# Performance work log

Hardware: AMD Instinct MI355X
Metric: run time of the kernel (lower is better)

## Reference

```python
import jax, jax.numpy as jnp
import numpy as np

DIM = 1024
HEADS = 16
DIM_HEAD = 64
INNER = HEADS * DIM_HEAD  # 1024
SCALE = DIM_HEAD ** -0.5


def setup_inputs() -> dict:
    key = jax.random.key(0)
    ks = jax.random.split(key, 5)
    B, N = 4, 2048
    x = jax.random.normal(ks[0], (B, N, DIM), dtype=jnp.float32)
    # torch Linear weights are [out, in]; store transposed [in, out] for x @ W
    s = 1.0 / np.sqrt(DIM)
    Wq = jax.random.uniform(ks[1], (DIM, INNER), minval=-s, maxval=s, dtype=jnp.float32)
    Wkv = jax.random.uniform(ks[2], (DIM, 2 * INNER), minval=-s, maxval=s, dtype=jnp.float32)
    so = 1.0 / np.sqrt(INNER)
    Wo = jax.random.uniform(ks[3], (INNER, DIM), minval=-so, maxval=so, dtype=jnp.float32)
    bo = jax.random.uniform(ks[4], (DIM,), minval=-so, maxval=so, dtype=jnp.float32)
    return {"x": x, "Wq": Wq, "Wkv": Wkv, "Wo": Wo, "bo": bo}


def reference(x, Wq, Wkv, Wo, bo):
    B, N, _ = x.shape
    q = x @ Wq                      # [B, N, INNER]
    kv = x @ Wkv                    # [B, N, 2*INNER]
    k, v = jnp.split(kv, 2, axis=-1)

    def split_heads(t):
        return t.reshape(B, N, HEADS, DIM_HEAD).transpose(0, 2, 1, 3)  # [B,H,N,D]

    q, k, v = split_heads(q) * SCALE, split_heads(k), split_heads(v)
    sim = jnp.einsum('bhid,bhjd->bhij', q, k)  # [B,H,N,N]
    mask_value = -jnp.finfo(sim.dtype).max
    # causal: mask strictly-upper triangle (triu with offset j-i+1 = 1)
    causal_mask = jnp.triu(jnp.ones((N, N), dtype=bool), k=1)
    sim = jnp.where(causal_mask[None, None, :, :], mask_value, sim)
    attn = jax.nn.softmax(sim, axis=-1)
    out = jnp.einsum('bhij,bhjd->bhid', attn, v)            # [B,H,N,D]
    out = out.transpose(0, 2, 1, 3).reshape(B, N, INNER)    # [B,N,INNER]
    return out @ Wo + bo
```

## Files before the change

kernel.cpp:

```cpp
#include <hip/hip_runtime.h>

typedef unsigned short u16;
typedef __bf16 bf16x8 __attribute__((ext_vector_type(8)));
typedef float floatx4 __attribute__((ext_vector_type(4)));
typedef unsigned as1_u32 __attribute__((address_space(1)));
typedef unsigned as3_u32 __attribute__((address_space(3)));

__device__ inline u16 f2bf(float f) {
    unsigned int u = __builtin_bit_cast(unsigned int, f);
    u += 0x7fffu + ((u >> 16) & 1u);
    return (u16)(u >> 16);
}
__device__ inline floatx4 mfma16(bf16x8 a, bf16x8 b, floatx4 c) {
    return __builtin_amdgcn_mfma_f32_16x16x32_bf16(a, b, c, 0, 0, 0);
}
__device__ inline void gld16(const u16* g, u16* l) {
    __builtin_amdgcn_global_load_lds((const as1_u32*)g, (as3_u32*)l, 16, 0, 0);
}
__device__ inline unsigned permpack(float lo, float hi) {
    return __builtin_amdgcn_perm(__builtin_bit_cast(unsigned, hi),
                                 __builtin_bit_cast(unsigned, lo), 0x07060302u);
}

#define NSEQ 2048
#define DIM  1024
#define HEADS 16
#define DHEAD 64
#define QSCALE 0.18033688f
#define CSHIFT 4.328085f

__device__ inline void transpose_tile(const float* __restrict__ src,
                                      u16* __restrict__ dst, int ncols,
                                      int n0, int k0, int t) {
    __shared__ u16 tile[64][72];
    #pragma unroll
    for (int rr = 0; rr < 4; rr++) {
        const int k = (t >> 4) + rr * 16;
        const int n = (t & 15) * 4;
        float4 v = *(const float4*)&src[(size_t)(k0 + k) * ncols + n0 + n];
        tile[n + 0][k] = f2bf(v.x); tile[n + 1][k] = f2bf(v.y);
        tile[n + 2][k] = f2bf(v.z); tile[n + 3][k] = f2bf(v.w);
    }
    __syncthreads();
    #pragma unroll
    for (int ww = 0; ww < 2; ww++) {
        const int idx = t + ww * 256;
        const int n = idx >> 3, g = idx & 7;
        u16 tmp[8] __attribute__((aligned(16)));
        #pragma unroll
        for (int i = 0; i < 8; i++) tmp[i] = tile[n][g * 8 + i];
        *(uint4*)&dst[(size_t)(n0 + n) * 1024 + k0 + g * 8] = *(const uint4*)tmp;
    }
}

__global__ __launch_bounds__(256) void prep_fused(
    const float* __restrict__ x,  u16* __restrict__ xb,
    const float* __restrict__ Wq, const float* __restrict__ Wkv,
    u16* __restrict__ Wt,
    const float* __restrict__ Wo, u16* __restrict__ WotF)
{
    const int bid = blockIdx.x;
    const int t = threadIdx.x;
    if (bid < 4096) {
        const size_t i = ((size_t)bid * 256 + t) * 8;
        float4 a = *(const float4*)&x[i];
        float4 b = *(const float4*)&x[i + 4];
        u16 o[8] __attribute__((aligned(16)));
        o[0] = f2bf(a.x); o[1] = f2bf(a.y); o[2] = f2bf(a.z); o[3] = f2bf(a.w);
        o[4] = f2bf(b.x); o[5] = f2bf(b.y); o[6] = f2bf(b.z); o[7] = f2bf(b.w);
        *(uint4*)&xb[i] = *(const uint4*)o;
    } else if (bid < 4352) {
        const int v = bid - 4096;
        transpose_tile(Wq, Wt, 1024, (v & 15) * 64, (v >> 4) * 64, t);
    } else if (bid < 4864) {
        const int v = bid - 4352;
        transpose_tile(Wkv, Wt + (size_t)1024 * 1024, 2048, (v & 31) * 64, (v >> 5) * 64, t);
    } else {
        const int v = bid - 4864;
        transpose_tile(Wo, WotF, 1024, (v & 15) * 64, (v >> 4) * 64, t);
    }
}

__global__ __launch_bounds__(256) void transpose_conv(const float* __restrict__ src,
                                                      u16* __restrict__ dst, int ncols) {
    transpose_tile(src, dst, ncols, blockIdx.x * 64, blockIdx.y * 64, threadIdx.x);
}

__global__ __launch_bounds__(256) void qkv_gemm_v6(
    const u16* __restrict__ xb, const u16* __restrict__ Wt,
    u16* __restrict__ q_ws, u16* __restrict__ k_ws, u16* __restrict__ v_ws)
{
    __shared__ u16 As[2][2][128 * 32];
    __shared__ u16 Bs[2][2][128 * 32];

    const int n0 = blockIdx.x * 128;
    const int m0 = blockIdx.y * 128;
    const int t = threadIdx.x, lane = t & 63, w = t >> 6;
    const int wr = w >> 1, wc = w & 1;
    const int quad = lane >> 4, l16 = lane & 15;
    const int lrow = lane >> 2;
    const int lk = (((lane & 3) ^ ((lane >> 3) & 3)) * 8);
    const int rsw = ((l16 >> 1) & 3);

    floatx4 acc[4][4];
    #pragma unroll
    for (int i = 0; i < 4; i++)
        #pragma unroll
        for (int j = 0; j < 4; j++) acc[i][j] = floatx4{0.f, 0.f, 0.f, 0.f};

#define STAGE_V6(kt, buf) do {                                             \
    const size_t k0s = (size_t)(kt) * 64;                                  \
    _Pragma("unroll")                                                      \
    for (int hh = 0; hh < 2; hh++) {                                       \
        const int row = w * 32 + hh * 16;                                  \
        const size_t ga = (size_t)(m0 + row + lrow) * DIM + k0s + lk;      \
        const size_t gb = (size_t)(n0 + row + lrow) * DIM + k0s + lk;      \
        gld16(&xb[ga],      &As[buf][0][row * 32]);                        \
        gld16(&xb[ga + 32], &As[buf][1][row * 32]);                        \
        gld16(&Wt[gb],      &Bs[buf][0][row * 32]);                        \
        gld16(&Wt[gb + 32], &Bs[buf][1][row * 32]);                        \
    }                                                                      \
} while (0)

    STAGE_V6(0, 0);
    STAGE_V6(1, 1);

    for (int kt = 0; kt < 16; kt++) {
        const int cur = kt & 1;
        if (kt < 15) asm volatile("s_waitcnt vmcnt(8)" ::: "memory");
        else         asm volatile("s_waitcnt vmcnt(0)" ::: "memory");
        __builtin_amdgcn_s_barrier();
        __builtin_amdgcn_sched_barrier(0);

        #pragma unroll
        for (int ks = 0; ks < 2; ks++) {
            const u16* al = &As[cur][ks][0];
            const u16* bl = &Bs[cur][ks][0];
            bf16x8 af[4], bf[4];
            #pragma unroll
            for (int i = 0; i < 4; i++)
                af[i] = *(const bf16x8*)&al[(wr * 64 + i * 16 + l16) * 32
                                            + ((quad ^ rsw) * 8)];
            #pragma unroll
            for (int j = 0; j < 4; j++)
                bf[j] = *(const bf16x8*)&bl[(wc * 64 + j * 16 + l16) * 32
                                            + ((quad ^ rsw) * 8)];
            __builtin_amdgcn_s_setprio(1);
            #pragma unroll
            for (int i = 0; i < 4; i++)
                #pragma unroll
                for (int j = 0; j < 4; j++)
                    acc[i][j] = mfma16(af[i], bf[j], acc[i][j]);
            __builtin_amdgcn_s_setprio(0);
        }

        __builtin_amdgcn_sched_barrier(0);
        __builtin_amdgcn_s_barrier();
        __builtin_amdgcn_sched_barrier(0);
        if (kt < 14) STAGE_V6(kt + 2, cur);
    }
#undef STAGE_V6

    const int seg = n0 >> 10;
    #pragma unroll
    for (int j = 0; j < 4; j++) {
        const int n  = n0 + wc * 64 + j * 16 + l16;
        const int nn = n & 1023;
        const int h  = nn >> 6, d = nn & 63;
        #pragma unroll
        for (int i = 0; i < 4; i++) {
            const int mb = m0 + wr * 64 + i * 16 + quad * 4;
            const int b = mb >> 11, ib = mb & (NSEQ - 1);
            if (seg == 0) {
                #pragma unroll
                for (int r = 0; r < 4; r++)
                    q_ws[(((size_t)(b * HEADS + h)) * NSEQ + ib + r) * DHEAD + d] =
                        f2bf(acc[i][j][r] * QSCALE);
            } else if (seg == 1) {
                #pragma unroll
                for (int r = 0; r < 4; r++)
                    k_ws[(((size_t)(b * HEADS + h)) * NSEQ + ib + r) * DHEAD + d] =
                        f2bf(acc[i][j][r]);
            } else {
                u16 tmp[4] __attribute__((aligned(8)));
                #pragma unroll
                for (int r = 0; r < 4; r++) tmp[r] = f2bf(acc[i][j][r]);
                *(uint2*)&v_ws[(((size_t)(b * HEADS + h)) * DHEAD + d) * NSEQ + ib] =
                    *(const uint2*)tmp;
            }
        }
    }
}

__global__ __launch_bounds__(256) void attn_v11(
    const u16* __restrict__ q_ws, const u16* __restrict__ k_ws,
    const u16* __restrict__ v_ws, u16* __restrict__ attn_ws)
{
    __shared__ u16 kds[2][64 * 64];
    __shared__ u16 vds[2][64 * 64];
    __shared__ u16 p_lds[4 * 1024];

    const int bid = blockIdx.x;
    const int bh  = bid & 63;
    const int pr  = bid >> 6;
    const int b   = bh >> 4, h = bh & 15;

    const u16* qb = q_ws + (size_t)bh * NSEQ * DHEAD;
    const u16* kb = k_ws + (size_t)bh * NSEQ * DHEAD;
    const u16* vb = v_ws + (size_t)bh * DHEAD * NSEQ;

    const int t    = threadIdx.x;
    const int lane = t & 63, w = t >> 6;
    const int quad = lane >> 4, l16 = lane & 15;

    const int srow8 = lane >> 3;
    const int chunk = (lane & 7) ^ srow8;
    const int krow  = w * 16 + srow8;
    const size_t koff = (size_t)krow * DHEAD + chunk * 8;
    const size_t voff = (size_t)krow * NSEQ + chunk * 8;
    u16* klbase = (u16*)&kds[0][0] + w * 1024;
    u16* vlbase = (u16*)&vds[0][0] + w * 1024;
    const int sw = (l16 & 7);

    bf16x8 ones;
    #pragma unroll
    for (int i = 0; i < 8; i++) ones[i] = (__bf16)1.0f;

    for (int seg = 0; seg < 2; seg++) {
        const int tq = seg ? pr : (31 - pr);
        const int i0 = tq * 64;
        const int jt_max = tq;

        bf16x8 qf[2];
        #pragma unroll
        for (int dg = 0; dg < 2; dg++)
            qf[dg] = *(const bf16x8*)&qb[(size_t)(i0 + w * 16 + l16) * DHEAD
                                         + dg * 32 + quad * 8];

        floatx4 lacc = floatx4{0.f, 0.f, 0.f, 0.f};
        floatx4 acc[4];
        #pragma unroll
        for (int dg = 0; dg < 4; dg++) acc[dg] = floatx4{0.f, 0.f, 0.f, 0.f};

        __syncthreads();
        gld16(&kb[koff],             klbase);
        gld16(&kb[koff + 8 * DHEAD], klbase + 512);
        gld16(&vb[voff],             vlbase);
        gld16(&vb[voff + 8 * NSEQ],  vlbase + 512);

        for (int jt = 0; jt <= jt_max; jt++) {
            const int cur = jt & 1;
            __syncthreads();

            if (jt < jt_max) {
                const size_t j64 = (size_t)(jt + 1) * 64;
                const int nb = (cur ^ 1) * 4096;
                gld16(&kb[j64 * DHEAD + koff],             klbase + nb);
                gld16(&kb[j64 * DHEAD + koff + 8 * DHEAD], klbase + nb + 512);
                gld16(&vb[j64 + voff],                     vlbase + nb);
                gld16(&vb[j64 + voff + 8 * NSEQ],          vlbase + nb + 512);
            }

            const u16* kl = &kds[cur][0];
            const u16* vl = &vds[cur][0];
            const int j0 = jt * 64;

            floatx4 s[4];
            #pragma unroll
            for (int g = 0; g < 4; g++)
                s[g] = floatx4{-CSHIFT, -CSHIFT, -CSHIFT, -CSHIFT};
            __builtin_amdgcn_s_setprio(1);
            #pragma unroll
            for (int dg = 0; dg < 2; dg++)
                #pragma unroll
                for (int g = 0; g < 4; g++) {
                    bf16x8 kf = *(const bf16x8*)&kl[(g * 16 + l16) * 64
                                                    + (((dg * 4 + quad) ^ sw) * 8)];
                    s[g] = mfma16(kf, qf[dg], s[g]);
                }
            __builtin_amdgcn_s_setprio(0);

            if (j0 + 63 > i0 + w * 16) {
                const int i = i0 + w * 16 + l16;
                #pragma unroll
                for (int g = 0; g < 4; g++) {
                    const int jb = j0 + g * 16 + quad * 4;
                    #pragma unroll
                    for (int r = 0; r < 4; r++)
                        if (jb + r > i) s[g][r] = -1e30f;
                }
            }

            #pragma unroll
            for (int g = 0; g < 4; g++) {
                #pragma unroll
                for (int r = 0; r < 4; r++)
                    s[g][r] = __builtin_amdgcn_exp2f(s[g][r]);
                uint2 pk;
                pk.x = permpack(s[g][0], s[g][1]);
                pk.y = permpack(s[g][2], s[g][3]);
                const int c = 2 * g + (quad >> 1);
                *(uint2*)&p_lds[w * 1024 + (c >> 2) * 512 + (c & 3) * 128
                                + l16 * 8 + (quad & 1) * 4] = pk;
            }
            asm volatile("s_waitcnt lgkmcnt(0)" ::: "memory");

            __builtin_amdgcn_s_setprio(1);
            #pragma unroll
            for (int jg = 0; jg < 2; jg++) {
                bf16x8 pf = *(const bf16x8*)&p_lds[w * 1024 + jg * 512
                                                   + quad * 128 + l16 * 8];
                lacc = mfma16(pf, ones, lacc);
                #pragma unroll
                for (int dg = 0; dg < 4; dg++) {
                    bf16x8 vf = *(const bf16x8*)&vl[(dg * 16 + l16) * 64
                                                    + (((jg * 4 + quad) ^ sw) * 8)];
                    acc[dg] = mfma16(pf, vf, acc[dg]);
                }
            }
            __builtin_amdgcn_s_setprio(0);
        }

        float linv[4];
        #pragma unroll
        for (int r = 0; r < 4; r++)
            linv[r] = 1.0f / lacc[r];
        #pragma unroll
        for (int dg = 0; dg < 4; dg++)
            #pragma unroll
            for (int r = 0; r < 4; r++) {
                const float o = acc[dg][r] * linv[r];
                const int i = i0 + w * 16 + quad * 4 + r;
                attn_ws[(((size_t)(b * NSEQ + i)) * HEADS + h) * DHEAD + dg * 16 + l16] =
                    f2bf(o);
            }
    }
}

__global__ __launch_bounds__(256) void out_gemm_v6(
    const u16* __restrict__ attn, const u16* __restrict__ Wot,
    const float* __restrict__ bo, float* __restrict__ out)
{
    __shared__ u16 As[2][2][128 * 32];
    __shared__ u16 Bs[2][2][128 * 32];

    const int n0 = blockIdx.x * 128;
    const int m0 = blockIdx.y * 128;
    const int t = threadIdx.x, lane = t & 63, w = t >> 6;
    const int wr = w >> 1, wc = w & 1;
    const int quad = lane >> 4, l16 = lane & 15;
    const int lrow = lane >> 2;
    const int lk = (((lane & 3) ^ ((lane >> 3) & 3)) * 8);
    const int rsw = ((l16 >> 1) & 3);

    floatx4 acc[4][4];
    #pragma unroll
    for (int i = 0; i < 4; i++)
        #pragma unroll
        for (int j = 0; j < 4; j++) acc[i][j] = floatx4{0.f, 0.f, 0.f, 0.f};

#define STAGE_O6(kt, buf) do {                                             \
    const size_t k0s = (size_t)(kt) * 64;                                  \
    _Pragma("unroll")                                                      \
    for (int hh = 0; hh < 2; hh++) {                                       \
        const int row = w * 32 + hh * 16;                                  \
        const size_t ga = (size_t)(m0 + row + lrow) * DIM + k0s + lk;      \
        const size_t gb = (size_t)(n0 + row + lrow) * DIM + k0s + lk;      \
        gld16(&attn[ga],      &As[buf][0][row * 32]);                      \
        gld16(&attn[ga + 32], &As[buf][1][row * 32]);                      \
        gld16(&Wot[gb],       &Bs[buf][0][row * 32]);                      \
        gld16(&Wot[gb + 32],  &Bs[buf][1][row * 32]);                      \
    }                                                                      \
} while (0)

    STAGE_O6(0, 0);
    STAGE_O6(1, 1);

    for (int kt = 0; kt < 16; kt++) {
        const int cur = kt & 1;
        if (kt < 15) asm volatile("s_waitcnt vmcnt(8)" ::: "memory");
        else         asm volatile("s_waitcnt vmcnt(0)" ::: "memory");
        __builtin_amdgcn_s_barrier();
        __builtin_amdgcn_sched_barrier(0);

        #pragma unroll
        for (int ks = 0; ks < 2; ks++) {
            const u16* al = &As[cur][ks][0];
            const u16* bl = &Bs[cur][ks][0];
            bf16x8 af[4], bf[4];
            #pragma unroll
            for (int i = 0; i < 4; i++)
                af[i] = *(const bf16x8*)&al[(wr * 64 + i * 16 + l16) * 32
                                            + ((quad ^ rsw) * 8)];
            #pragma unroll
            for (int j = 0; j < 4; j++)
                bf[j] = *(const bf16x8*)&bl[(wc * 64 + j * 16 + l16) * 32
                                            + ((quad ^ rsw) * 8)];
            __builtin_amdgcn_s_setprio(1);
            #pragma unroll
            for (int i = 0; i < 4; i++)
                #pragma unroll
                for (int j = 0; j < 4; j++)
                    acc[i][j] = mfma16(af[i], bf[j], acc[i][j]);
            __builtin_amdgcn_s_setprio(0);
        }

        __builtin_amdgcn_sched_barrier(0);
        __builtin_amdgcn_s_barrier();
        __builtin_amdgcn_sched_barrier(0);
        if (kt < 14) STAGE_O6(kt + 2, cur);
    }
#undef STAGE_O6

    #pragma unroll
    for (int j = 0; j < 4; j++) {
        const int n = n0 + wc * 64 + j * 16 + l16;
        const float bias = bo[n];
        #pragma unroll
        for (int i = 0; i < 4; i++) {
            #pragma unroll
            for (int r = 0; r < 4; r++) {
                const int m = m0 + wr * 64 + i * 16 + quad * 4 + r;
                out[(size_t)m * DIM + n] = acc[i][j][r] + bias;
            }
        }
    }
}

extern "C" void kernel_launch(void* const* d_in, const int* in_sizes, int n_in,
                              void* d_out, int out_size, void* d_ws, size_t ws_size,
                              hipStream_t stream) {
    const float* x   = (const float*)d_in[0];
    const float* Wq  = (const float*)d_in[1];
    const float* Wkv = (const float*)d_in[2];
    const float* Wo  = (const float*)d_in[3];
    const float* bo  = (const float*)d_in[4];

    u16* q_ws = (u16*)d_out;
    u16* xb   = (u16*)d_out + (size_t)8388608;

    u16* ws   = (u16*)d_ws;
    u16* k_ws = ws;
    u16* v_ws = ws + (size_t)8388608;
    u16* a_ws = ws + (size_t)16777216;
    u16* Wt   = a_ws;

    const bool fuse_wo = ws_size >= (size_t)50 * 1024 * 1024;
    u16* Wot = fuse_wo ? ws + (size_t)25165824 : k_ws;

    prep_fused<<<fuse_wo ? 5120 : 4864, 256, 0, stream>>>(
        x, xb, Wq, Wkv, Wt, Wo, Wot);
    qkv_gemm_v6<<<dim3(24, 64), 256, 0, stream>>>(xb, Wt, q_ws, k_ws, v_ws);
    attn_v11<<<dim3(1024), 256, 0, stream>>>(q_ws, k_ws, v_ws, a_ws);
    if (!fuse_wo)
        transpose_conv<<<dim3(16, 16), 256, 0, stream>>>(Wo, Wot, 1024);
    out_gemm_v6<<<dim3(8, 64), 256, 0, stream>>>(a_ws, Wot, bo, (float*)d_out);
}
```

Before: 242.8 us.

## Process both causal query tiles in one pass sharing K/V tile loads

```diff
diff --git a/kernel.cpp b/kernel.cpp
--- a/kernel.cpp
+++ b/kernel.cpp
@@ -192,7 +192,7 @@
     }
 }
 
-__global__ __launch_bounds__(256) void attn_v11(
+__global__ __launch_bounds__(256, 4) void attn_v12(
     const u16* __restrict__ q_ws, const u16* __restrict__ k_ws,
     const u16* __restrict__ v_ws, u16* __restrict__ attn_ws)
 {
@@ -202,7 +202,7 @@
 
     const int bid = blockIdx.x;
     const int bh  = bid & 63;
-    const int pr  = bid >> 6;
+    const int p   = bid >> 6;
     const int b   = bh >> 4, h = bh & 15;
 
     const u16* qb = q_ws + (size_t)bh * NSEQ * DHEAD;
@@ -226,79 +226,126 @@
     #pragma unroll
     for (int i = 0; i < 8; i++) ones[i] = (__bf16)1.0f;
 
-    for (int seg = 0; seg < 2; seg++) {
-        const int tq = seg ? pr : (31 - pr);
-        const int i0 = tq * 64;
-        const int jt_max = tq;
-
-        bf16x8 qf[2];
+    const int tqA = 31 - p;
+    const int i0A = tqA * 64;
+    const int i0B = p * 64;
+
+    bf16x8 qfA[2], qfB[2];
+    #pragma unroll
+    for (int dg = 0; dg < 2; dg++) {
+        qfA[dg] = *(const bf16x8*)&qb[(size_t)(i0A + w * 16 + l16) * DHEAD
+                                      + dg * 32 + quad * 8];
+        qfB[dg] = *(const bf16x8*)&qb[(size_t)(i0B + w * 16 + l16) * DHEAD
+                                      + dg * 32 + quad * 8];
+    }
+
+    floatx4 laccA = floatx4{0.f,0.f,0.f,0.f}, laccB = floatx4{0.f,0.f,0.f,0.f};
+    floatx4 accA[4], accB[4];
+    #pragma unroll
+    for (int dg = 0; dg < 4; dg++) {
+        accA[dg] = floatx4{0.f, 0.f, 0.f, 0.f};
+        accB[dg] = floatx4{0.f, 0.f, 0.f, 0.f};
+    }
+
+    gld16(&kb[koff],             klbase);
+    gld16(&kb[koff + 8 * DHEAD], klbase + 512);
+    gld16(&vb[voff],             vlbase);
+    gld16(&vb[voff + 8 * NSEQ],  vlbase + 512);
+
+    for (int jt = 0; jt <= tqA; jt++) {
+        const int cur = jt & 1;
+        __syncthreads();
+
+        if (jt < tqA) {
+            const size_t j64 = (size_t)(jt + 1) * 64;
+            const int nb = (cur ^ 1) * 4096;
+            gld16(&kb[j64 * DHEAD + koff],             klbase + nb);
+            gld16(&kb[j64 * DHEAD + koff + 8 * DHEAD], klbase + nb + 512);
+            gld16(&vb[j64 + voff],                     vlbase + nb);
+            gld16(&vb[j64 + voff + 8 * NSEQ],          vlbase + nb + 512);
+        }
+
+        const u16* kl = &kds[cur][0];
+        const u16* vl = &vds[cur][0];
+        const int j0 = jt * 64;
+        const bool dob = (jt <= p);
+
+        floatx4 sA[4], sB[4];
+        #pragma unroll
+        for (int g = 0; g < 4; g++) {
+            sA[g] = floatx4{-CSHIFT, -CSHIFT, -CSHIFT, -CSHIFT};
+            sB[g] = floatx4{-CSHIFT, -CSHIFT, -CSHIFT, -CSHIFT};
+        }
+        __builtin_amdgcn_s_setprio(1);
         #pragma unroll
         for (int dg = 0; dg < 2; dg++)
-            qf[dg] = *(const bf16x8*)&qb[(size_t)(i0 + w * 16 + l16) * DHEAD
-                                         + dg * 32 + quad * 8];
-
-        floatx4 lacc = floatx4{0.f, 0.f, 0.f, 0.f};
-        floatx4 acc[4];
-        #pragma unroll
-        for (int dg = 0; dg < 4; dg++) acc[dg] = floatx4{0.f, 0.f, 0.f, 0.f};
-
-        __syncthreads();
-        gld16(&kb[koff],             klbase);
-        gld16(&kb[koff + 8 * DHEAD], klbase + 512);
-        gld16(&vb[voff],             vlbase);
-        gld16(&vb[voff + 8 * NSEQ],  vlbase + 512);
-
-        for (int jt = 0; jt <= jt_max; jt++) {
-            const int cur = jt & 1;
-            __syncthreads();
-
-            if (jt < jt_max) {
-                const size_t j64 = (size_t)(jt + 1) * 64;
-                const int nb = (cur ^ 1) * 4096;
-                gld16(&kb[j64 * DHEAD + koff],             klbase + nb);
-                gld16(&kb[j64 * DHEAD + koff + 8 * DHEAD], klbase + nb + 512);
-                gld16(&vb[j64 + voff],                     vlbase + nb);
-                gld16(&vb[j64 + voff + 8 * NSEQ],          vlbase + nb + 512);
-            }
-
-            const u16* kl = &kds[cur][0];
-            const u16* vl = &vds[cur][0];
-            const int j0 = jt * 64;
-
-            floatx4 s[4];
-            #pragma unroll
-            for (int g = 0; g < 4; g++)
-                s[g] = floatx4{-CSHIFT, -CSHIFT, -CSHIFT, -CSHIFT};
-            __builtin_amdgcn_s_setprio(1);
-            #pragma unroll
-            for (int dg = 0; dg < 2; dg++)
-                #pragma unroll
-                for (int g = 0; g < 4; g++) {
-                    bf16x8 kf = *(const bf16x8*)&kl[(g * 16 + l16) * 64
-                                                    + (((dg * 4 + quad) ^ sw) * 8)];
-                    s[g] = mfma16(kf, qf[dg], s[g]);
-                }
-            __builtin_amdgcn_s_setprio(0);
-
-            if (j0 + 63 > i0 + w * 16) {
-                const int i = i0 + w * 16 + l16;
+            #pragma unroll
+            for (int g = 0; g < 4; g++) {
+                bf16x8 kf = *(const bf16x8*)&kl[(g * 16 + l16) * 64
+                                                + (((dg * 4 + quad) ^ sw) * 8)];
+                sA[g] = mfma16(kf, qfA[dg], sA[g]);
+                if (dob) sB[g] = mfma16(kf, qfB[dg], sB[g]);
+            }
+        __builtin_amdgcn_s_setprio(0);
+
+        if (j0 + 63 > i0A + w * 16) {
+            const int i = i0A + w * 16 + l16;
+            #pragma unroll
+            for (int g = 0; g < 4; g++) {
+                const int jb = j0 + g * 16 + quad * 4;
+                #pragma unroll
+                for (int r = 0; r < 4; r++)
+                    if (jb + r > i) sA[g][r] = -1e30f;
+            }
+        }
+        #pragma unroll
+        for (int g = 0; g < 4; g++) {
+            #pragma unroll
+            for (int r = 0; r < 4; r++)
+                sA[g][r] = __builtin_amdgcn_exp2f(sA[g][r]);
+            uint2 pk;
+            pk.x = permpack(sA[g][0], sA[g][1]);
+            pk.y = permpack(sA[g][2], sA[g][3]);
+            const int c = 2 * g + (quad >> 1);
+            *(uint2*)&p_lds[w * 1024 + (c >> 2) * 512 + (c & 3) * 128
+                            + l16 * 8 + (quad & 1) * 4] = pk;
+        }
+        asm volatile("s_waitcnt lgkmcnt(0)" ::: "memory");
+
+        __builtin_amdgcn_s_setprio(1);
+        #pragma unroll
+        for (int jg = 0; jg < 2; jg++) {
+            bf16x8 pf = *(const bf16x8*)&p_lds[w * 1024 + jg * 512
+                                               + quad * 128 + l16 * 8];
+            laccA = mfma16(pf, ones, laccA);
+            #pragma unroll
+            for (int dg = 0; dg < 4; dg++) {
+                bf16x8 vf = *(const bf16x8*)&vl[(dg * 16 + l16) * 64
+                                                + (((jg * 4 + quad) ^ sw) * 8)];
+                accA[dg] = mfma16(pf, vf, accA[dg]);
+            }
+        }
+        __builtin_amdgcn_s_setprio(0);
+
+        if (dob) {
+            if (j0 + 63 > i0B + w * 16) {
+                const int i = i0B + w * 16 + l16;
                 #pragma unroll
                 for (int g = 0; g < 4; g++) {
                     const int jb = j0 + g * 16 + quad * 4;
                     #pragma unroll
                     for (int r = 0; r < 4; r++)
-                        if (jb + r > i) s[g][r] = -1e30f;
+                        if (jb + r > i) sB[g][r] = -1e30f;
                 }
             }
-
             #pragma unroll
             for (int g = 0; g < 4; g++) {
                 #pragma unroll
                 for (int r = 0; r < 4; r++)
-                    s[g][r] = __builtin_amdgcn_exp2f(s[g][r]);
+                    sB[g][r] = __builtin_amdgcn_exp2f(sB[g][r]);
                 uint2 pk;
-                pk.x = permpack(s[g][0], s[g][1]);
-                pk.y = permpack(s[g][2], s[g][3]);
+                pk.x = permpack(sB[g][0], sB[g][1]);
+                pk.y = permpack(sB[g][2], sB[g][3]);
                 const int c = 2 * g + (quad >> 1);
                 *(uint2*)&p_lds[w * 1024 + (c >> 2) * 512 + (c & 3) * 128
                                 + l16 * 8 + (quad & 1) * 4] = pk;
@@ -310,27 +357,42 @@
             for (int jg = 0; jg < 2; jg++) {
                 bf16x8 pf = *(const bf16x8*)&p_lds[w * 1024 + jg * 512
                                                    + quad * 128 + l16 * 8];
-                lacc = mfma16(pf, ones, lacc);
+                laccB = mfma16(pf, ones, laccB);
                 #pragma unroll
                 for (int dg = 0; dg < 4; dg++) {
                     bf16x8 vf = *(const bf16x8*)&vl[(dg * 16 + l16) * 64
                                                     + (((jg * 4 + quad) ^ sw) * 8)];
-                    acc[dg] = mfma16(pf, vf, acc[dg]);
+                    accB[dg] = mfma16(pf, vf, accB[dg]);
                 }
             }
             __builtin_amdgcn_s_setprio(0);
         }
-
+    }
+
+    {
         float linv[4];
         #pragma unroll
-        for (int r = 0; r < 4; r++)
-            linv[r] = 1.0f / lacc[r];
+        for (int r = 0; r < 4; r++) linv[r] = 1.0f / laccA[r];
         #pragma unroll
         for (int dg = 0; dg < 4; dg++)
             #pragma unroll
             for (int r = 0; r < 4; r++) {
-                const float o = acc[dg][r] * linv[r];
-                const int i = i0 + w * 16 + quad * 4 + r;
+                const float o = accA[dg][r] * linv[r];
+                const int i = i0A + w * 16 + quad * 4 + r;
+                attn_ws[(((size_t)(b * NSEQ + i)) * HEADS + h) * DHEAD + dg * 16 + l16] =
+                    f2bf(o);
+            }
+    }
+    {
+        float linv[4];
+        #pragma unroll
+        for (int r = 0; r < 4; r++) linv[r] = 1.0f / laccB[r];
+        #pragma unroll
+        for (int dg = 0; dg < 4; dg++)
+            #pragma unroll
+            for (int r = 0; r < 4; r++) {
+                const float o = accB[dg][r] * linv[r];
+                const int i = i0B + w * 16 + quad * 4 + r;
                 attn_ws[(((size_t)(b * NSEQ + i)) * HEADS + h) * DHEAD + dg * 16 + l16] =
                     f2bf(o);
             }
@@ -451,7 +513,7 @@
     prep_fused<<<fuse_wo ? 5120 : 4864, 256, 0, stream>>>(
         x, xb, Wq, Wkv, Wt, Wo, Wot);
     qkv_gemm_v6<<<dim3(24, 64), 256, 0, stream>>>(xb, Wt, q_ws, k_ws, v_ws);
-    attn_v11<<<dim3(1024), 256, 0, stream>>>(q_ws, k_ws, v_ws, a_ws);
+    attn_v12<<<dim3(1024), 256, 0, stream>>>(q_ws, k_ws, v_ws, a_ws);
     if (!fuse_wo)
         transpose_conv<<<dim3(16, 16), 256, 0, stream>>>(Wo, Wot, 1024);
     out_gemm_v6<<<dim3(8, 64), 256, 0, stream>>>(a_ws, Wot, bo, (float*)d_out);
```

Result: slower. 313.9 us (+29.3%).
